# Optimization experiments

Hardware: AMD Instinct MI355X
Metric: run time of the kernel (lower is better)

Reference implementation:

```python
import jax, jax.numpy as jnp
import numpy as np
import math

B = 2048
INPUT_SIZE = 1024
OUTPUT_SIZE = 512
SPONGE = 1024
ACT = 256
REC = 256
STORE = ACT + REC  # 512
DEPTH = 8
BDEPTH = 10
NEUTRAL_C = 1.0
SQRT2 = math.sqrt(2.0)


def _make_structure():
    # Deterministic stand-in for the module's random.sample-based recall wiring.
    rng = np.random.RandomState(0)
    half = (SPONGE + 1) // 2
    shuffle_perm = np.array([i // 2 + (i % 2) * half for i in range(SPONGE)], dtype=np.int64)
    unused = []
    recall = []
    for i in range(DEPTH):
        unused.extend(range(i * STORE, (i + 1) * STORE))
        sel = rng.choice(len(unused), size=REC, replace=False)
        sel_set = set(sel.tolist())
        recall.append([unused[k] for k in sorted(sel_set)])
        unused = [u for k, u in enumerate(unused) if k not in sel_set]
    out_mem = np.array(sorted(unused), dtype=np.int64)  # 2048 leftover memory columns
    bf_size = len(out_mem) + SPONGE  # 3072
    bf_depth = int(math.ceil(math.log2(bf_size)))  # 12
    bf_half = (bf_size + 1) // 2
    bf_perm = np.array([i // 2 + (i % 2) * bf_half for i in range(bf_size)], dtype=np.int64)
    return shuffle_perm, np.array(recall, dtype=np.int64), out_mem, bf_perm, bf_size, bf_depth


def setup_inputs() -> dict:
    key = jax.random.key(0)
    ks = jax.random.split(key, 6)
    shuffle_perm, recall_idx, out_mem_idx, bf_perm, bf_size, bf_depth = _make_structure()
    return {
        "X": jax.random.normal(ks[0], (B, INPUT_SIZE), jnp.float32),
        "scales": jnp.ones((INPUT_SIZE,), jnp.float32),
        "angles": jax.random.uniform(ks[1], (DEPTH, BDEPTH, SPONGE // 2), jnp.float32) * (2 * math.pi),
        "act_bias": jax.random.normal(ks[2], (DEPTH, ACT), jnp.float32),
        "act_activation": jax.random.normal(ks[3], (DEPTH, ACT), jnp.float32),
        "act_curvature": jax.random.normal(ks[4], (DEPTH, ACT), jnp.float32),
        "bf_angles": jax.random.uniform(ks[5], (bf_depth, bf_size // 2), jnp.float32) * (2 * math.pi),
        "shuffle_perm": jnp.asarray(shuffle_perm),
        "recall_idx": jnp.asarray(recall_idx),
        "output_mem_idx": jnp.asarray(out_mem_idx),
        "bf_perm": jnp.asarray(bf_perm),
    }


def _base_activation(x, c):
    # In the source, `a` is overwritten with torch.tensor(1.0), so a == 1.
    t = (math.pi / 4) / c
    y0 = (1.0 / c) * (1.0 / SQRT2 - math.cos(math.pi / 2))  # = 1/(c*sqrt(2))
    m0 = math.sin(math.pi / 2)  # = 1
    y1 = (1.0 / c) * (1.0 / SQRT2 - 1.0)
    m1 = math.sin(0.0)  # = 0
    mid = (1.0 / c) * (1.0 / SQRT2 - jnp.cos(math.pi / 4 + c * x))
    return jnp.where(x > t, y0 + m0 * (x - t), jnp.where(x < -t, y1 + m1 * (x + t), mid))


def _butterfly(x, angles, perm):
    # angles: [n_layers, exch]; shuffle -> Givens rotation per pair, extra passthrough
    exch = angles.shape[1]
    for j in range(angles.shape[0]):
        s = x[:, perm]
        x1, x2 = s[:, :exch], s[:, exch:2 * exch]
        ca, sa = jnp.cos(angles[j]), jnp.sin(angles[j])
        x = jnp.concatenate([ca * x1 + sa * x2, -sa * x1 + ca * x2, s[:, 2 * exch:]], axis=1)
    return x


def reference(X, scales, angles, act_bias, act_activation, act_curvature, bf_angles,
              shuffle_perm, recall_idx, output_mem_idx, bf_perm):
    Xs = X * scales
    sponge = Xs[:, :SPONGE]  # input_size == sponge_size: no zero pad, memory[0] is empty
    mem = jnp.zeros((Xs.shape[0], DEPTH * STORE), Xs.dtype)
    for i in range(DEPTH):
        sponge = _butterfly(sponge, angles[i], shuffle_perm)
        x1 = sponge[:, STORE:STORE + ACT] + act_bias[i]  # activation_position == store_size
        c = 0.5 * NEUTRAL_C * (act_curvature[i] + jnp.sqrt(act_curvature[i] ** 2 + 1.0))
        ap = _base_activation(x1, c)
        am = _base_activation(-x1, c)
        act_out = jnp.stack([ap, am], axis=2).reshape(ap.shape[0], 2 * ACT)  # interleave +/-
        mem = mem.at[:, i * STORE:(i + 1) * STORE].set(sponge[:, :STORE])
        recall = mem[:, recall_idx[i]]  # indices only address already-filled columns
        # [act_out | sponge[store:act_pos] (empty) | sponge[act_pos+ACT:] | recall]
        sponge = jnp.concatenate([act_out, sponge[:, STORE + ACT:], recall], axis=1)
    pre = jnp.concatenate([mem[:, output_mem_idx], sponge], axis=1)  # [B, 3072]
    out = _butterfly(pre, bf_angles, bf_perm)
    return out[:, :OUTPUT_SIZE]
```

## Files before the change

kernel.cpp:

```cpp
#include <hip/hip_runtime.h>
#include <math.h>

#define NB 2048
#define DEPTH 8

#define FTAB_OFF    0
#define BF01_OFF    81920
#define BFF_OFF     88064
#define ACT4_OFF    98304
#define PHYS_OFF    106496
#define PHYSR_OFF   110592
#define PHYSO2_OFF  112640

__global__ void tab_precompute(const float* __restrict__ angles,
                               const float* __restrict__ bf_angles,
                               const float* __restrict__ act_bias,
                               const float* __restrict__ act_curv,
                               float* __restrict__ ws) {
    int id = blockIdx.x * 256 + threadIdx.x;
    if (id < 40960) {
        int w  = id & 3;
        int t  = (id >> 2) & 255;
        int dg = id >> 10;
        int d = dg / 5, g = dg - 5 * d;
        int a = 2 * (t & 127) + (t >> 7);
        int pair = (w == 0) ? a : (w == 1) ? (a + 256)
                 : (w == 2) ? (2 * a) : (2 * a + 1);
        int st = 2 * g + (w >> 1);
        float ang = angles[(d * 10 + st) * 512 + pair];
        float s, c; sincosf(ang, &s, &c);
        ws[FTAB_OFF + 2 * id]     = c;
        ws[FTAB_OFF + 2 * id + 1] = s;
    } else if (id < 44032) {
        int e = id - 40960;
        int w = e & 3; int ti = e >> 2;
        int t = ti / 3; int i = ti - 3 * t;
        int a = t + 256 * i;
        int pair = (w == 0) ? a : (w == 1) ? (a + 768)
                 : (w == 2) ? (2 * a) : (2 * a + 1);
        int stage = (w < 2) ? 0 : 1;
        float ang = bf_angles[stage * 1536 + pair];
        float s, c; sincosf(ang, &s, &c);
        ws[BF01_OFF + 2 * e]     = c;
        ws[BF01_OFF + 2 * e + 1] = s;
    } else if (id < 49152) {
        int e = id - 44032;
        int f = e >> 10; int rem = e & 1023; int t = rem >> 2; int w = rem & 3;
        int P;
        if (f == 0) P = 3 * t;
        else { int k = 8 - 2 * f; P = ((t >> (2 * f)) * (768 >> k)) + (t & ((256 >> k) - 1)); }
        int pair = (w == 0) ? P : (w == 1) ? (P + 768)
                 : (w == 2) ? (2 * P) : (2 * P + 1);
        int stage = (w < 2) ? (2 + 2 * f) : (3 + 2 * f);
        float ang = bf_angles[stage * 1536 + pair];
        float s, c; sincosf(ang, &s, &c);
        ws[BFF_OFF + 2 * e]     = c;
        ws[BFF_OFF + 2 * e + 1] = s;
    } else if (id < 51200) {
        int ida = id - 49152;
        float cu = act_curv[ida];
        float c  = 0.5f * (cu + sqrtf(cu * cu + 1.0f));
        ((float4*)(ws + ACT4_OFF))[ida] =
            make_float4(act_bias[ida], c, 1.0f / c, 0.0f);
    }
}

__global__ void phys_precompute(const int* __restrict__ recall_idx,
                                const int* __restrict__ out_mem_idx,
                                float* __restrict__ ws) {
    __shared__ int physL[4096];
    int t = threadIdx.x;
    for (int q = 0; q < 4; ++q) {
        int v = t + q * 1024;
        int p;
        for (;;) {
            int d = v >> 9, j = v & 511;
            if (d == 0)  { p = j; break; }
            if (j < 256) { p = 256 + d * 256 + j; break; }
            v = recall_idx[(d - 1) * 256 + (j - 256)];
        }
        physL[t + q * 1024] = p;
        ((int*)(ws + PHYS_OFF))[t + q * 1024] = p;
    }
    __syncthreads();
    for (int q = 0; q < 2; ++q) {
        int i = t + q * 1024;
        ((int*)(ws + PHYSR_OFF))[i] = physL[recall_idx[i]];
    }
    for (int e = t; e < 3072; e += 1024) {
        int tt = e / 12; int r = e - 12 * tt; int i = r >> 2; int k = r & 3;
        int a = tt + 256 * i;
        int tl = a >> 1, th = a & 1;
        int pos = tl + 1536 * th + 384 * k;
        int val = (pos < 2048) ? physL[out_mem_idx[pos]] : (2304 + (pos - 2048));
        ((int*)(ws + PHYSO2_OFF))[e] = val;
    }
}

__device__ __forceinline__ float actf(float x, float c, float ic) {
    const float is2 = 0.70710678118654752f;
    float tt = 0.78539816339744831f * ic;
    float y0 = is2 * ic;
    float y1 = (is2 - 1.0f) * ic;
    float mid = ic * (is2 - __cosf(0.78539816339744831f + c * x));
    return x > tt ? (y0 + (x - tt)) : (x < -tt ? y1 : mid);
}

__device__ __forceinline__ int swz(int p) {
    return (p & 1) | ((p & 0x3C) >> 1) | ((((p >> 6) ^ (p >> 1)) & 1) << 5)
         | (((p >> 1) & 1) << 6) | (p & 0x380);
}

__launch_bounds__(256, 4)
__global__ void sponge_kernel(const float* __restrict__ X,
                              const float* __restrict__ scales,
                              const float* __restrict__ ws,
                              float* __restrict__ out) {
    __shared__ float lds[8704];
    float* L0 = lds;
    float* L1 = lds + 4352;
    const int t = threadIdx.x;
    const int rowA = blockIdx.x * 2;

    const float4* bf01  = (const float4*)(ws + BF01_OFF);
    const float4* bff   = (const float4*)(ws + BFF_OFF);
    const float4* act4  = (const float4*)(ws + ACT4_OFF);
    const int* phys   = (const int*)(ws + PHYS_OFF);
    const int* physr  = (const int*)(ws + PHYSR_OFF);
    const int* physo2 = (const int*)(ws + PHYSO2_OFF);

    const int tl = t & 127, th = t >> 7;
    const int b  = tl + th * 512;
    const int a  = 2 * tl + th;

    const int wA0 = swz(2 * a), wA1 = swz(2 * a + 512);
    const int rd0 = swz(b), rd1 = swz(b + 128), rd2 = swz(b + 256), rd3 = swz(b + 384);
    const int zmem = swz(2 * t);
    const int u = t - 128;
    int za0 = 0, za1 = 0, za2 = 0, za3 = 0, zk0 = 0, zk1 = 0;
    if (t < 128) {
        int k0 = t >> 1;
        za0 = swz(512 + k0);       za1 = swz(512 + k0 + 64);
        za2 = swz(512 + k0 + 128); za3 = swz(512 + k0 + 192);
    } else {
        zk0 = swz(768 + u); zk1 = swz(896 + u);
    }

    float hA0, hA1, hA2, hA3, hB0, hB1, hB2, hB3;
    {
        const float* Xr0 = X + (size_t)rowA * 1024;
        const float* Xr1 = Xr0 + 1024;
        float s0 = scales[b], s1 = scales[b + 128], s2 = scales[b + 256], s3 = scales[b + 384];
        hA0 = Xr0[b] * s0; hA1 = Xr0[b + 128] * s1;
        hA2 = Xr0[b + 256] * s2; hA3 = Xr0[b + 384] * s3;
        hB0 = Xr1[b] * s0; hB1 = Xr1[b + 128] * s1;
        hB2 = Xr1[b + 256] * s2; hB3 = Xr1[b + 384] * s3;
    }

    int woff = 2304, roff = 3328;
    const float4* ft = (const float4*)(ws + FTAB_OFF) + 2 * t;

    for (int d = 0; d < DEPTH; ++d) {
        for (int g = 0; g < 5; ++g) {
            float4 csA = ft[0], csB = ft[1]; ft += 512;
            float g0 =  csA.x * hA0 + csA.y * hA2;
            float g2 = -csA.y * hA0 + csA.x * hA2;
            float g1 =  csA.z * hA1 + csA.w * hA3;
            float g3 = -csA.w * hA1 + csA.z * hA3;
            float fA0 =  csB.x * g0 + csB.y * g1;
            float fA2 = -csB.y * g0 + csB.x * g1;
            float fA1 =  csB.z * g2 + csB.w * g3;
            float fA3 = -csB.w * g2 + csB.z * g3;
            float G0 =  csA.x * hB0 + csA.y * hB2;
            float G2 = -csA.y * hB0 + csA.x * hB2;
            float G1 =  csA.z * hB1 + csA.w * hB3;
            float G3 = -csA.w * hB1 + csA.z * hB3;
            float fB0 =  csB.x * G0 + csB.y * G1;
            float fB2 = -csB.y * G0 + csB.x * G1;
            float fB1 =  csB.z * G2 + csB.w * G3;
            float fB3 = -csB.w * G2 + csB.z * G3;
            *(float2*)(L0 + woff + wA0) = make_float2(fA0, fA1);
            *(float2*)(L0 + woff + wA1) = make_float2(fA2, fA3);
            *(float2*)(L1 + woff + wA0) = make_float2(fB0, fB1);
            *(float2*)(L1 + woff + wA1) = make_float2(fB2, fB3);
            { int tmp = woff; woff = roff; roff = tmp; }
            __syncthreads();
            if (g < 4) {
                hA0 = L0[roff + rd0]; hA1 = L0[roff + rd1];
                hA2 = L0[roff + rd2]; hA3 = L0[roff + rd3];
                hB0 = L1[roff + rd0]; hB1 = L1[roff + rd1];
                hB2 = L1[roff + rd2]; hB3 = L1[roff + rd3];
            }
        }
        const float* z0 = L0 + roff;
        const float* z1 = L1 + roff;
        float2 mvA = *(const float2*)(z0 + zmem);
        float2 mvB = *(const float2*)(z1 + zmem);
        int2 pm = ((const int2*)(phys + d * 512))[t];
        L0[pm.x] = mvA.x; L0[pm.y] = mvA.y;
        L1[pm.x] = mvB.x; L1[pm.y] = mvB.y;
        int r0 = 0, r1 = 0;
        if (t < 128) {
            int k0 = t >> 1;
            float4 a0 = act4[d * 256 + k0];
            float4 a1 = act4[d * 256 + k0 + 64];
            float4 a2 = act4[d * 256 + k0 + 128];
            float4 a3 = act4[d * 256 + k0 + 192];
            float sgn = (t & 1) ? -1.0f : 1.0f;
            hA0 = actf(sgn * (z0[za0] + a0.x), a0.y, a0.z);
            hA1 = actf(sgn * (z0[za1] + a1.x), a1.y, a1.z);
            hA2 = actf(sgn * (z0[za2] + a2.x), a2.y, a2.z);
            hA3 = actf(sgn * (z0[za3] + a3.x), a3.y, a3.z);
            hB0 = actf(sgn * (z1[za0] + a0.x), a0.y, a0.z);
            hB1 = actf(sgn * (z1[za1] + a1.x), a1.y, a1.z);
            hB2 = actf(sgn * (z1[za2] + a2.x), a2.y, a2.z);
            hB3 = actf(sgn * (z1[za3] + a3.x), a3.y, a3.z);
        } else {
            hA0 = z0[zk0]; hA1 = z0[zk1];
            hB0 = z1[zk0]; hB1 = z1[zk1];
            r0 = physr[d * 256 + u];
            r1 = physr[d * 256 + u + 128];
        }
        __syncthreads();
        if (t >= 128) {
            hA2 = L0[r0]; hA3 = L0[r1];
            hB2 = L1[r0]; hB3 = L1[r1];
        }
    }

    L0[2304 + b] = hA0; L0[2304 + b + 128] = hA1;
    L0[2304 + b + 256] = hA2; L0[2304 + b + 384] = hA3;
    L1[2304 + b] = hB0; L1[2304 + b + 128] = hB1;
    L1[2304 + b + 256] = hB2; L1[2304 + b + 384] = hB3;
    __syncthreads();

    float vA0, vA1, vA2, vA3, vA4, vA5, vA6, vA7, vA8, vA9, vA10, vA11;
    float vB0, vB1, vB2, vB3, vB4, vB5, vB6, vB7, vB8, vB9, vB10, vB11;
    {
        int4 pg = ((const int4*)(physo2 + t * 12))[0];
        vA0 = L0[pg.x]; vA1 = L0[pg.y]; vA2 = L0[pg.z]; vA3 = L0[pg.w];
        vB0 = L1[pg.x]; vB1 = L1[pg.y]; vB2 = L1[pg.z]; vB3 = L1[pg.w];
        pg = ((const int4*)(physo2 + t * 12))[1];
        vA4 = L0[pg.x]; vA5 = L0[pg.y]; vA6 = L0[pg.z]; vA7 = L0[pg.w];
        vB4 = L1[pg.x]; vB5 = L1[pg.y]; vB6 = L1[pg.z]; vB7 = L1[pg.w];
        pg = ((const int4*)(physo2 + t * 12))[2];
        vA8 = L0[pg.x]; vA9 = L0[pg.y]; vA10 = L0[pg.z]; vA11 = L0[pg.w];
        vB8 = L1[pg.x]; vB9 = L1[pg.y]; vB10 = L1[pg.z]; vB11 = L1[pg.w];
    }
    __syncthreads();

#define BF01_STEP(i, qA0, qA1, qA2, qA3, qB0, qB1, qB2, qB3)                        \
    {                                                                               \
        float4 c01 = bf01[(t * 3 + (i)) * 2];                                       \
        float4 c23 = bf01[(t * 3 + (i)) * 2 + 1];                                   \
        float g0 =  c01.x * qA0 + c01.y * qA2;                                      \
        float g2 = -c01.y * qA0 + c01.x * qA2;                                      \
        float g1 =  c01.z * qA1 + c01.w * qA3;                                      \
        float g3 = -c01.w * qA1 + c01.z * qA3;                                      \
        float y0 =  c23.x * g0 + c23.y * g1;                                        \
        float y2 = -c23.y * g0 + c23.x * g1;                                        \
        float y1 =  c23.z * g2 + c23.w * g3;                                        \
        float y3 = -c23.w * g2 + c23.z * g3;                                        \
        *(float2*)(L0 + 2 * t + 512 * (i))        = make_float2(y0, y1);            \
        *(float2*)(L0 + 2 * t + 512 * (i) + 1536) = make_float2(y2, y3);            \
        g0 =  c01.x * qB0 + c01.y * qB2;                                            \
        g2 = -c01.y * qB0 + c01.x * qB2;                                            \
        g1 =  c01.z * qB1 + c01.w * qB3;                                            \
        g3 = -c01.w * qB1 + c01.z * qB3;                                            \
        y0 =  c23.x * g0 + c23.y * g1;                                              \
        y2 = -c23.y * g0 + c23.x * g1;                                              \
        y1 =  c23.z * g2 + c23.w * g3;                                              \
        y3 = -c23.w * g2 + c23.z * g3;                                              \
        *(float2*)(L1 + 2 * t + 512 * (i))        = make_float2(y0, y1);            \
        *(float2*)(L1 + 2 * t + 512 * (i) + 1536) = make_float2(y2, y3);            \
    }
    BF01_STEP(0, vA0, vA1, vA2, vA3, vB0, vB1, vB2, vB3)
    BF01_STEP(1, vA4, vA5, vA6, vA7, vB4, vB5, vB6, vB7)
    BF01_STEP(2, vA8, vA9, vA10, vA11, vB8, vB9, vB10, vB11)
#undef BF01_STEP
    __syncthreads();

#pragma unroll
    for (int f = 0; f < 4; ++f) {
        int P;
        if (f == 0) P = 3 * t;
        else { const int k = 8 - 2 * f;
               P = ((t >> (2 * f)) * (768 >> k)) + (t & ((256 >> k) - 1)); }
        int base = (P >> 1) + (P & 1) * 1536;
        float4 csS = bff[(f * 256 + t) * 2];
        float4 csT = bff[(f * 256 + t) * 2 + 1];
        float xA1p = L0[base], xA1q = L0[base + 384];
        float xA2p = L0[base + 768], xA2q = L0[base + 1152];
        float xB1p = L1[base], xB1q = L1[base + 384];
        float xB2p = L1[base + 768], xB2q = L1[base + 1152];
        float o1P =  csS.x * xA1p + csS.y * xA2p;
        float o2P = -csS.y * xA1p + csS.x * xA2p;
        float o1Q =  csS.z * xA1q + csS.w * xA2q;
        float o2Q = -csS.w * xA1q + csS.z * xA2q;
        float yA0 =  csT.x * o1P + csT.y * o1Q;
        float yA2 = -csT.y * o1P + csT.x * o1Q;
        float yA1 =  csT.z * o2P + csT.w * o2Q;
        float yA3 = -csT.w * o2P + csT.z * o2Q;
        o1P =  csS.x * xB1p + csS.y * xB2p;
        o2P = -csS.y * xB1p + csS.x * xB2p;
        o1Q =  csS.z * xB1q + csS.w * xB2q;
        o2Q = -csS.w * xB1q + csS.z * xB2q;
        float yB0 =  csT.x * o1P + csT.y * o1Q;
        float yB2 = -csT.y * o1P + csT.x * o1Q;
        float yB1 =  csT.z * o2P + csT.w * o2Q;
        float yB3 = -csT.w * o2P + csT.z * o2Q;
        __syncthreads();
        *(float2*)(L0 + 2 * P)        = make_float2(yA0, yA1);
        *(float2*)(L0 + 2 * P + 1536) = make_float2(yA2, yA3);
        *(float2*)(L1 + 2 * P)        = make_float2(yB0, yB1);
        *(float2*)(L1 + 2 * P + 1536) = make_float2(yB2, yB3);
        __syncthreads();
    }

    {
        int base = (t >> 1) + (t & 1) * 1536;
        float4 csS = bff[(4 * 256 + t) * 2];
        float4 csT = bff[(4 * 256 + t) * 2 + 1];
        float x1p = L0[base], x1q = L0[base + 384];
        float x2p = L0[base + 768], x2q = L0[base + 1152];
        float o1P =  csS.x * x1p + csS.y * x2p;
        float o2P = -csS.y * x1p + csS.x * x2p;
        float o1Q =  csS.z * x1q + csS.w * x2q;
        float o2Q = -csS.w * x1q + csS.z * x2q;
        *(float2*)(out + (size_t)rowA * 512 + 2 * t) =
            make_float2(csT.x * o1P + csT.y * o1Q, csT.z * o2P + csT.w * o2Q);
        x1p = L1[base]; x1q = L1[base + 384];
        x2p = L1[base + 768]; x2q = L1[base + 1152];
        o1P =  csS.x * x1p + csS.y * x2p;
        o2P = -csS.y * x1p + csS.x * x2p;
        o1Q =  csS.z * x1q + csS.w * x2q;
        o2Q = -csS.w * x1q + csS.z * x2q;
        *(float2*)(out + (size_t)(rowA + 1) * 512 + 2 * t) =
            make_float2(csT.x * o1P + csT.y * o1Q, csT.z * o2P + csT.w * o2Q);
    }
}

extern "C" void kernel_launch(void* const* d_in, const int* in_sizes, int n_in,
                              void* d_out, int out_size, void* d_ws, size_t ws_size,
                              hipStream_t stream) {
    const float* X          = (const float*)d_in[0];
    const float* scales     = (const float*)d_in[1];
    const float* angles     = (const float*)d_in[2];
    const float* act_bias   = (const float*)d_in[3];
    const float* act_curv   = (const float*)d_in[5];
    const float* bf_angles  = (const float*)d_in[6];
    const int*   recall_idx  = (const int*)d_in[8];
    const int*   out_mem_idx = (const int*)d_in[9];

    float* ws = (float*)d_ws;

    tab_precompute<<<200, 256, 0, stream>>>(angles, bf_angles, act_bias, act_curv, ws);
    phys_precompute<<<1, 1024, 0, stream>>>(recall_idx, out_mem_idx, ws);
    sponge_kernel<<<NB / 2, 256, 0, stream>>>(X, scales, ws, (float*)d_out);
}
```

Measured before the change: 122.3 us.

## Merge setup kernels, simplify LDS swizzle, fuse memory scatter into last butterfly group

Merges the two precompute kernels into one launch, with one extra block handling the physical-index tables. The LDS swizzle becomes a simpler XOR layout, so the butterfly exchange writes a single float4 per row. In the last group of each depth, results are scattered straight to their physical memory slots, with the recall loads issued before one barrier. This removes a separate memory-copy phase and one __syncthreads per depth, at the cost of more index tables and possible bank conflicts in the new layout.

New measurement: 122.3 us. About the same (-0.0%).

```diff
diff --git a/kernel.cpp b/kernel.cpp
--- a/kernel.cpp
+++ b/kernel.cpp
@@ -8,92 +8,96 @@
 #define BF01_OFF    81920
 #define BFF_OFF     88064
 #define ACT4_OFF    98304
-#define PHYS_OFF    106496
+#define PHYSA_OFF   106496
 #define PHYSR_OFF   110592
 #define PHYSO2_OFF  112640
 
-__global__ void tab_precompute(const float* __restrict__ angles,
-                               const float* __restrict__ bf_angles,
-                               const float* __restrict__ act_bias,
-                               const float* __restrict__ act_curv,
-                               float* __restrict__ ws) {
-    int id = blockIdx.x * 256 + threadIdx.x;
-    if (id < 40960) {
-        int w  = id & 3;
-        int t  = (id >> 2) & 255;
-        int dg = id >> 10;
-        int d = dg / 5, g = dg - 5 * d;
-        int a = 2 * (t & 127) + (t >> 7);
-        int pair = (w == 0) ? a : (w == 1) ? (a + 256)
-                 : (w == 2) ? (2 * a) : (2 * a + 1);
-        int st = 2 * g + (w >> 1);
-        float ang = angles[(d * 10 + st) * 512 + pair];
-        float s, c; sincosf(ang, &s, &c);
-        ws[FTAB_OFF + 2 * id]     = c;
-        ws[FTAB_OFF + 2 * id + 1] = s;
-    } else if (id < 44032) {
-        int e = id - 40960;
-        int w = e & 3; int ti = e >> 2;
-        int t = ti / 3; int i = ti - 3 * t;
-        int a = t + 256 * i;
-        int pair = (w == 0) ? a : (w == 1) ? (a + 768)
-                 : (w == 2) ? (2 * a) : (2 * a + 1);
-        int stage = (w < 2) ? 0 : 1;
-        float ang = bf_angles[stage * 1536 + pair];
-        float s, c; sincosf(ang, &s, &c);
-        ws[BF01_OFF + 2 * e]     = c;
-        ws[BF01_OFF + 2 * e + 1] = s;
-    } else if (id < 49152) {
-        int e = id - 44032;
-        int f = e >> 10; int rem = e & 1023; int t = rem >> 2; int w = rem & 3;
-        int P;
-        if (f == 0) P = 3 * t;
-        else { int k = 8 - 2 * f; P = ((t >> (2 * f)) * (768 >> k)) + (t & ((256 >> k) - 1)); }
-        int pair = (w == 0) ? P : (w == 1) ? (P + 768)
-                 : (w == 2) ? (2 * P) : (2 * P + 1);
-        int stage = (w < 2) ? (2 + 2 * f) : (3 + 2 * f);
-        float ang = bf_angles[stage * 1536 + pair];
-        float s, c; sincosf(ang, &s, &c);
-        ws[BFF_OFF + 2 * e]     = c;
-        ws[BFF_OFF + 2 * e + 1] = s;
-    } else if (id < 51200) {
-        int ida = id - 49152;
-        float cu = act_curv[ida];
-        float c  = 0.5f * (cu + sqrtf(cu * cu + 1.0f));
-        ((float4*)(ws + ACT4_OFF))[ida] =
-            make_float4(act_bias[ida], c, 1.0f / c, 0.0f);
-    }
-}
-
-__global__ void phys_precompute(const int* __restrict__ recall_idx,
-                                const int* __restrict__ out_mem_idx,
-                                float* __restrict__ ws) {
+__global__ void setup_kernel(const float* __restrict__ angles,
+                             const float* __restrict__ bf_angles,
+                             const float* __restrict__ act_bias,
+                             const float* __restrict__ act_curv,
+                             const int* __restrict__ recall_idx,
+                             const int* __restrict__ out_mem_idx,
+                             float* __restrict__ ws) {
     __shared__ int physL[4096];
-    int t = threadIdx.x;
-    for (int q = 0; q < 4; ++q) {
-        int v = t + q * 1024;
-        int p;
-        for (;;) {
-            int d = v >> 9, j = v & 511;
-            if (d == 0)  { p = j; break; }
-            if (j < 256) { p = 256 + d * 256 + j; break; }
-            v = recall_idx[(d - 1) * 256 + (j - 256)];
-        }
-        physL[t + q * 1024] = p;
-        ((int*)(ws + PHYS_OFF))[t + q * 1024] = p;
-    }
-    __syncthreads();
-    for (int q = 0; q < 2; ++q) {
-        int i = t + q * 1024;
-        ((int*)(ws + PHYSR_OFF))[i] = physL[recall_idx[i]];
-    }
-    for (int e = t; e < 3072; e += 1024) {
-        int tt = e / 12; int r = e - 12 * tt; int i = r >> 2; int k = r & 3;
-        int a = tt + 256 * i;
-        int tl = a >> 1, th = a & 1;
-        int pos = tl + 1536 * th + 384 * k;
-        int val = (pos < 2048) ? physL[out_mem_idx[pos]] : (2304 + (pos - 2048));
-        ((int*)(ws + PHYSO2_OFF))[e] = val;
+    if (blockIdx.x < 200) {
+        int id = blockIdx.x * 256 + threadIdx.x;
+        if (id < 40960) {
+            int w = id & 3, t = (id >> 2) & 255, dg = id >> 10;
+            int d = dg / 5, g = dg - 5 * d;
+            int a = 2 * (t & 127) + (t >> 7);
+            int pair = (w == 0) ? a : (w == 1) ? (a + 256)
+                     : (w == 2) ? (2 * a) : (2 * a + 1);
+            int st = 2 * g + (w >> 1);
+            float ang = angles[(d * 10 + st) * 512 + pair];
+            float s, c; sincosf(ang, &s, &c);
+            ws[FTAB_OFF + 2 * id]     = c;
+            ws[FTAB_OFF + 2 * id + 1] = s;
+        } else if (id < 44032) {
+            int e = id - 40960;
+            int w = e & 3; int ti = e >> 2;
+            int t = ti / 3; int i = ti - 3 * t;
+            int a = t + 256 * i;
+            int pair = (w == 0) ? a : (w == 1) ? (a + 768)
+                     : (w == 2) ? (2 * a) : (2 * a + 1);
+            int stage = (w < 2) ? 0 : 1;
+            float ang = bf_angles[stage * 1536 + pair];
+            float s, c; sincosf(ang, &s, &c);
+            ws[BF01_OFF + 2 * e]     = c;
+            ws[BF01_OFF + 2 * e + 1] = s;
+        } else if (id < 49152) {
+            int e = id - 44032;
+            int f = e >> 10; int rem = e & 1023; int t = rem >> 2; int w = rem & 3;
+            int P;
+            if (f == 0) P = 3 * t;
+            else if (f < 4) { int k = 8 - 2 * f;
+                              P = ((t >> (2 * f)) * (768 >> k)) + (t & ((256 >> k) - 1)); }
+            else P = t;
+            int pair = (w == 0) ? P : (w == 1) ? (P + 768)
+                     : (w == 2) ? (2 * P) : (2 * P + 1);
+            int stage = (w < 2) ? (2 + 2 * f) : (3 + 2 * f);
+            float ang = bf_angles[stage * 1536 + pair];
+            float s, c; sincosf(ang, &s, &c);
+            ws[BFF_OFF + 2 * e]     = c;
+            ws[BFF_OFF + 2 * e + 1] = s;
+        } else if (id < 51200) {
+            int ida = id - 49152;
+            float cu = act_curv[ida];
+            float c  = 0.5f * (cu + sqrtf(cu * cu + 1.0f));
+            ((float4*)(ws + ACT4_OFF))[ida] =
+                make_float4(act_bias[ida], c, 1.0f / c, 0.0f);
+        }
+    } else {
+        int tid = threadIdx.x;
+        for (int e = tid; e < 4096; e += 256) {
+            int v = e, p;
+            for (;;) {
+                int d = v >> 9, j = v & 511;
+                if (d == 0)  { p = j; break; }
+                if (j < 256) { p = 256 + d * 256 + j; break; }
+                v = recall_idx[(d - 1) * 256 + (j - 256)];
+            }
+            physL[e] = p;
+        }
+        __syncthreads();
+        int* pa = (int*)(ws + PHYSA_OFF);
+        for (int e = tid; e < 2048; e += 256) {
+            int d = e >> 8, t = e & 255;
+            int a = 2 * (t & 127) + (t >> 7);
+            pa[2 * e]     = physL[d * 512 + 2 * a];
+            pa[2 * e + 1] = physL[d * 512 + 2 * a + 1];
+        }
+        int* pr = (int*)(ws + PHYSR_OFF);
+        for (int e = tid; e < 2048; e += 256)
+            pr[e] = physL[recall_idx[e]];
+        int* po = (int*)(ws + PHYSO2_OFF);
+        for (int e = tid; e < 3072; e += 256) {
+            int tt = e / 12; int r = e - 12 * tt; int i = r >> 2; int k = r & 3;
+            int a = tt + 256 * i;
+            int tl2 = a >> 1, th2 = a & 1;
+            int pos = tl2 + 1536 * th2 + 384 * k;
+            po[e] = (pos < 2048) ? physL[out_mem_idx[pos]] : 2304 + (pos - 2048);
+        }
     }
 }
 
@@ -106,10 +110,7 @@
     return x > tt ? (y0 + (x - tt)) : (x < -tt ? y1 : mid);
 }
 
-__device__ __forceinline__ int swz(int p) {
-    return (p & 1) | ((p & 0x3C) >> 1) | ((((p >> 6) ^ (p >> 1)) & 1) << 5)
-         | (((p >> 1) & 1) << 6) | (p & 0x380);
-}
+__device__ __forceinline__ int xf(int A) { return A ^ (((A >> 7) & 1) << 2); }
 
 __launch_bounds__(256, 4)
 __global__ void sponge_kernel(const float* __restrict__ X,
@@ -125,32 +126,32 @@
     const float4* bf01  = (const float4*)(ws + BF01_OFF);
     const float4* bff   = (const float4*)(ws + BFF_OFF);
     const float4* act4  = (const float4*)(ws + ACT4_OFF);
-    const int* phys   = (const int*)(ws + PHYS_OFF);
-    const int* physr  = (const int*)(ws + PHYSR_OFF);
-    const int* physo2 = (const int*)(ws + PHYSO2_OFF);
+    const int2* physA  = (const int2*)(ws + PHYSA_OFF);
+    const int*  physr  = (const int*)(ws + PHYSR_OFF);
+    const int*  physo2 = (const int*)(ws + PHYSO2_OFF);
 
     const int tl = t & 127, th = t >> 7;
     const int b  = tl + th * 512;
     const int a  = 2 * tl + th;
 
-    const int wA0 = swz(2 * a), wA1 = swz(2 * a + 512);
-    const int rd0 = swz(b), rd1 = swz(b + 128), rd2 = swz(b + 256), rd3 = swz(b + 384);
-    const int zmem = swz(2 * t);
-    const int u = t - 128;
-    int za0 = 0, za1 = 0, za2 = 0, za3 = 0, zk0 = 0, zk1 = 0;
+    const int wq = xf(4 * a);
+    const int rb = xf(4 * (tl >> 1) + (tl & 1) + 2 * th);
+    const int u  = t - 128;
+    int za0 = 0, za1 = 0, za2 = 0, za3 = 0, kb = 0;
     if (t < 128) {
         int k0 = t >> 1;
-        za0 = swz(512 + k0);       za1 = swz(512 + k0 + 64);
-        za2 = swz(512 + k0 + 128); za3 = swz(512 + k0 + 192);
+        int zb = 4 * (k0 >> 1) + (k0 & 1) + 2;
+        za0 = xf(zb); za1 = xf(zb + 128); za2 = xf(zb + 256); za3 = xf(zb + 384);
     } else {
-        zk0 = swz(768 + u); zk1 = swz(896 + u);
+        kb = xf(512 + 4 * (u >> 1) + 2 + (u & 1));
     }
 
     float hA0, hA1, hA2, hA3, hB0, hB1, hB2, hB3;
     {
         const float* Xr0 = X + (size_t)rowA * 1024;
         const float* Xr1 = Xr0 + 1024;
-        float s0 = scales[b], s1 = scales[b + 128], s2 = scales[b + 256], s3 = scales[b + 384];
+        float s0 = scales[b], s1 = scales[b + 128];
+        float s2 = scales[b + 256], s3 = scales[b + 384];
         hA0 = Xr0[b] * s0; hA1 = Xr0[b + 128] * s1;
         hA2 = Xr0[b + 256] * s2; hA3 = Xr0[b + 384] * s3;
         hB0 = Xr1[b] * s0; hB1 = Xr1[b + 128] * s1;
@@ -160,71 +161,70 @@
     int woff = 2304, roff = 3328;
     const float4* ft = (const float4*)(ws + FTAB_OFF) + 2 * t;
 
+#define DQUAD(cA, cB, i0, i1, i2, i3, F0, F1, F2, F3)                    \
+    { float g0 =  (cA).x * (i0) + (cA).y * (i2);                         \
+      float g2 = -(cA).y * (i0) + (cA).x * (i2);                         \
+      float g1 =  (cA).z * (i1) + (cA).w * (i3);                         \
+      float g3 = -(cA).w * (i1) + (cA).z * (i3);                         \
+      F0 =  (cB).x * g0 + (cB).y * g1;                                   \
+      F2 = -(cB).y * g0 + (cB).x * g1;                                   \
+      F1 =  (cB).z * g2 + (cB).w * g3;                                   \
+      F3 = -(cB).w * g2 + (cB).z * g3; }
+
     for (int d = 0; d < DEPTH; ++d) {
         for (int g = 0; g < 5; ++g) {
             float4 csA = ft[0], csB = ft[1]; ft += 512;
-            float g0 =  csA.x * hA0 + csA.y * hA2;
-            float g2 = -csA.y * hA0 + csA.x * hA2;
-            float g1 =  csA.z * hA1 + csA.w * hA3;
-            float g3 = -csA.w * hA1 + csA.z * hA3;
-            float fA0 =  csB.x * g0 + csB.y * g1;
-            float fA2 = -csB.y * g0 + csB.x * g1;
-            float fA1 =  csB.z * g2 + csB.w * g3;
-            float fA3 = -csB.w * g2 + csB.z * g3;
-            float G0 =  csA.x * hB0 + csA.y * hB2;
-            float G2 = -csA.y * hB0 + csA.x * hB2;
-            float G1 =  csA.z * hB1 + csA.w * hB3;
-            float G3 = -csA.w * hB1 + csA.z * hB3;
-            float fB0 =  csB.x * G0 + csB.y * G1;
-            float fB2 = -csB.y * G0 + csB.x * G1;
-            float fB1 =  csB.z * G2 + csB.w * G3;
-            float fB3 = -csB.w * G2 + csB.z * G3;
-            *(float2*)(L0 + woff + wA0) = make_float2(fA0, fA1);
-            *(float2*)(L0 + woff + wA1) = make_float2(fA2, fA3);
-            *(float2*)(L1 + woff + wA0) = make_float2(fB0, fB1);
-            *(float2*)(L1 + woff + wA1) = make_float2(fB2, fB3);
-            { int tmp = woff; woff = roff; roff = tmp; }
-            __syncthreads();
+            float fA0, fA1, fA2, fA3, fB0, fB1, fB2, fB3;
+            DQUAD(csA, csB, hA0, hA1, hA2, hA3, fA0, fA1, fA2, fA3);
+            DQUAD(csA, csB, hB0, hB1, hB2, hB3, fB0, fB1, fB2, fB3);
             if (g < 4) {
-                hA0 = L0[roff + rd0]; hA1 = L0[roff + rd1];
-                hA2 = L0[roff + rd2]; hA3 = L0[roff + rd3];
-                hB0 = L1[roff + rd0]; hB1 = L1[roff + rd1];
-                hB2 = L1[roff + rd2]; hB3 = L1[roff + rd3];
+                *(float4*)(L0 + woff + wq) = make_float4(fA0, fA1, fA2, fA3);
+                *(float4*)(L1 + woff + wq) = make_float4(fB0, fB1, fB2, fB3);
+                { int tmp = woff; woff = roff; roff = tmp; }
+                __syncthreads();
+                const float* e0 = L0 + roff + rb;
+                const float* e1 = L1 + roff + rb;
+                hA0 = e0[0]; hA1 = e0[256]; hA2 = e0[512]; hA3 = e0[768];
+                hB0 = e1[0]; hB1 = e1[256]; hB2 = e1[512]; hB3 = e1[768];
+            } else {
+                int2 pm = physA[d * 256 + t];
+                L0[pm.x] = fA0; L0[pm.y] = fA1;
+                L1[pm.x] = fB0; L1[pm.y] = fB1;
+                *(float2*)(L0 + woff + wq + 2) = make_float2(fA2, fA3);
+                *(float2*)(L1 + woff + wq + 2) = make_float2(fB2, fB3);
+                { int tmp = woff; woff = roff; roff = tmp; }
+                int r0 = 0, r1 = 0;
+                float4 a0, a1, a2, a3;
+                if (t < 128) {
+                    int k0 = t >> 1;
+                    a0 = act4[d * 256 + k0];
+                    a1 = act4[d * 256 + k0 + 64];
+                    a2 = act4[d * 256 + k0 + 128];
+                    a3 = act4[d * 256 + k0 + 192];
+                } else {
+                    r0 = physr[d * 256 + u];
+                    r1 = physr[d * 256 + u + 128];
+                }
+                __syncthreads();
+                const float* z0 = L0 + roff;
+                const float* z1 = L1 + roff;
+                if (t < 128) {
+                    float sgn = (t & 1) ? -1.0f : 1.0f;
+                    hA0 = actf(sgn * (z0[za0] + a0.x), a0.y, a0.z);
+                    hA1 = actf(sgn * (z0[za1] + a1.x), a1.y, a1.z);
+                    hA2 = actf(sgn * (z0[za2] + a2.x), a2.y, a2.z);
+                    hA3 = actf(sgn * (z0[za3] + a3.x), a3.y, a3.z);
+                    hB0 = actf(sgn * (z1[za0] + a0.x), a0.y, a0.z);
+                    hB1 = actf(sgn * (z1[za1] + a1.x), a1.y, a1.z);
+                    hB2 = actf(sgn * (z1[za2] + a2.x), a2.y, a2.z);
+                    hB3 = actf(sgn * (z1[za3] + a3.x), a3.y, a3.z);
+                } else {
+                    hA0 = z0[kb]; hA1 = z0[kb + 256];
+                    hB0 = z1[kb]; hB1 = z1[kb + 256];
+                    hA2 = L0[r0]; hA3 = L0[r1];
+                    hB2 = L1[r0]; hB3 = L1[r1];
+                }
             }
-        }
-        const float* z0 = L0 + roff;
-        const float* z1 = L1 + roff;
-        float2 mvA = *(const float2*)(z0 + zmem);
-        float2 mvB = *(const float2*)(z1 + zmem);
-        int2 pm = ((const int2*)(phys + d * 512))[t];
-        L0[pm.x] = mvA.x; L0[pm.y] = mvA.y;
-        L1[pm.x] = mvB.x; L1[pm.y] = mvB.y;
-        int r0 = 0, r1 = 0;
-        if (t < 128) {
-            int k0 = t >> 1;
-            float4 a0 = act4[d * 256 + k0];
-            float4 a1 = act4[d * 256 + k0 + 64];
-            float4 a2 = act4[d * 256 + k0 + 128];
-            float4 a3 = act4[d * 256 + k0 + 192];
-            float sgn = (t & 1) ? -1.0f : 1.0f;
-            hA0 = actf(sgn * (z0[za0] + a0.x), a0.y, a0.z);
-            hA1 = actf(sgn * (z0[za1] + a1.x), a1.y, a1.z);
-            hA2 = actf(sgn * (z0[za2] + a2.x), a2.y, a2.z);
-            hA3 = actf(sgn * (z0[za3] + a3.x), a3.y, a3.z);
-            hB0 = actf(sgn * (z1[za0] + a0.x), a0.y, a0.z);
-            hB1 = actf(sgn * (z1[za1] + a1.x), a1.y, a1.z);
-            hB2 = actf(sgn * (z1[za2] + a2.x), a2.y, a2.z);
-            hB3 = actf(sgn * (z1[za3] + a3.x), a3.y, a3.z);
-        } else {
-            hA0 = z0[zk0]; hA1 = z0[zk1];
-            hB0 = z1[zk0]; hB1 = z1[zk1];
-            r0 = physr[d * 256 + u];
-            r1 = physr[d * 256 + u + 128];
-        }
-        __syncthreads();
-        if (t >= 128) {
-            hA2 = L0[r0]; hA3 = L0[r1];
-            hB2 = L1[r0]; hB3 = L1[r1];
         }
     }
 
@@ -253,24 +253,11 @@
     {                                                                               \
         float4 c01 = bf01[(t * 3 + (i)) * 2];                                       \
         float4 c23 = bf01[(t * 3 + (i)) * 2 + 1];                                   \
-        float g0 =  c01.x * qA0 + c01.y * qA2;                                      \
-        float g2 = -c01.y * qA0 + c01.x * qA2;                                      \
-        float g1 =  c01.z * qA1 + c01.w * qA3;                                      \
-        float g3 = -c01.w * qA1 + c01.z * qA3;                                      \
-        float y0 =  c23.x * g0 + c23.y * g1;                                        \
-        float y2 = -c23.y * g0 + c23.x * g1;                                        \
-        float y1 =  c23.z * g2 + c23.w * g3;                                        \
-        float y3 = -c23.w * g2 + c23.z * g3;                                        \
+        float y0, y1, y2, y3;                                                       \
+        DQUAD(c01, c23, qA0, qA1, qA2, qA3, y0, y1, y2, y3);                        \
         *(float2*)(L0 + 2 * t + 512 * (i))        = make_float2(y0, y1);            \
         *(float2*)(L0 + 2 * t + 512 * (i) + 1536) = make_float2(y2, y3);            \
-        g0 =  c01.x * qB0 + c01.y * qB2;                                            \
-        g2 = -c01.y * qB0 + c01.x * qB2;                                            \
-        g1 =  c01.z * qB1 + c01.w * qB3;                                            \
-        g3 = -c01.w * qB1 + c01.z * qB3;                                            \
-        y0 =  c23.x * g0 + c23.y * g1;                                              \
-        y2 = -c23.y * g0 + c23.x * g1;                                              \
-        y1 =  c23.z * g2 + c23.w * g3;                                              \
-        y3 = -c23.w * g2 + c23.z * g3;                                              \
+        DQUAD(c01, c23, qB0, qB1, qB2, qB3, y0, y1, y2, y3);                        \
         *(float2*)(L1 + 2 * t + 512 * (i))        = make_float2(y0, y1);            \
         *(float2*)(L1 + 2 * t + 512 * (i) + 1536) = make_float2(y2, y3);            \
     }
@@ -338,6 +325,7 @@
         *(float2*)(out + (size_t)(rowA + 1) * 512 + 2 * t) =
             make_float2(csT.x * o1P + csT.y * o1Q, csT.z * o2P + csT.w * o2Q);
     }
+#undef DQUAD
 }
 
 extern "C" void kernel_launch(void* const* d_in, const int* in_sizes, int n_in,
@@ -354,7 +342,7 @@
 
     float* ws = (float*)d_ws;
 
-    tab_precompute<<<200, 256, 0, stream>>>(angles, bf_angles, act_bias, act_curv, ws);
-    phys_precompute<<<1, 1024, 0, stream>>>(recall_idx, out_mem_idx, ws);
+    setup_kernel<<<201, 256, 0, stream>>>(angles, bf_angles, act_bias, act_curv,
+                                          recall_idx, out_mem_idx, ws);
     sponge_kernel<<<NB / 2, 256, 0, stream>>>(X, scales, ws, (float*)d_out);
 }
```
